# Performance work log

Hardware: AMD Instinct MI355X
Metric: run time of the kernel (lower is better)

Reference implementation:

```python
import jax, jax.numpy as jnp
import numpy as np

jax.config.update("jax_enable_x64", True)

STRIDE = 1
PADDING = 1


def _im2col(x, k, s):
    # x: (n, c, H, W) already padded. Returns (n, c*k*k, oh*ow) with
    # channel-major, then (kh, kw) ordering -- matching torch unfold/img2col.
    n, c, H, W = x.shape
    oh = (H - k) // s + 1
    ow = (W - k) // s + 1
    # k*k = 9 slices: small fixed loop over kernel offsets, fully vectorized
    # over batch/channel/spatial dims.
    patches = jnp.stack(
        [x[:, :, i:i + s * (oh - 1) + 1:s, j:j + s * (ow - 1) + 1:s]
         for i in range(k) for j in range(k)],
        axis=2,
    )  # (n, c, k*k, oh, ow)
    return patches.reshape(n, c * k * k, oh * ow)


def setup_inputs() -> dict:
    key = jax.random.key(0)
    k1, k2, k3 = jax.random.split(key, 3)
    x = jax.random.randint(k1, (32, 64, 56, 56), 0, 65536, dtype=jnp.int64)
    weight = jax.random.randint(k2, (64, 64, 3, 3), 0, 65536, dtype=jnp.int64)
    bias = jax.random.randint(k3, (64,), 0, 65536, dtype=jnp.int64)
    return {"x": x, "weight": weight, "bias": bias}


def reference(x, weight, bias):
    kN, kC, k, _ = weight.shape
    n, c, H, W = x.shape
    oh = (H - k + 2 * PADDING) // STRIDE + 1
    ow = (W - k + 2 * PADDING) // STRIDE + 1
    # pad spatial dims with zeros (ring zero)
    xp = jnp.pad(x, ((0, 0), (0, 0), (PADDING, PADDING), (PADDING, PADDING)))
    cols = _im2col(xp, k, STRIDE)              # (n, c*k*k, L)
    cols_t = cols.transpose(0, 2, 1)           # (n, L, c*k*k)
    w2 = weight.reshape(kN, kC * k * k).T      # (c*k*k, kN)
    # int64 matmul: overflow wraps (two's complement), matching ring Z_{2^64}
    out = jnp.einsum('nlk,ko->nlo', cols_t, w2) + bias  # (n, L, kN)
    return out.transpose(0, 2, 1).reshape(n, kN, oh, ow)
```

## Files before the change

kernel.cpp:

```cpp
#include <hip/hip_runtime.h>


typedef int v4i __attribute__((ext_vector_type(4)));

#define XP   (58 * 58 * 128)
#define ROWB (58 * 128)
#define LCOL 144
#define LROW (58 * LCOL)

__device__ __align__(16) unsigned char g_xp[32 * XP];
__device__ int g_sp[32 * 3364];
__device__ __align__(16) unsigned char g_wb[2 * 9 * 64 * 64];
__device__ unsigned g_off[64];

__global__ __launch_bounds__(256) void packx(const int* __restrict__ x) {
    int gid = blockIdx.x * 256 + threadIdx.x;
    if (gid >= 32 * 3364) return;
    int p = gid % 3364;
    int n = gid / 3364;
    int pr = p / 58, pc = p - pr * 58;
    int ih = pr - 1, iw = pc - 1;
    unsigned char* ob = g_xp + (long)n * XP + (long)p * 128;
    int S;
    if ((unsigned)ih < 56u && (unsigned)iw < 56u) {
        const int* xp = x + (long)n * 64 * 3136 + ih * 56 + iw;
        unsigned lo[16], hi[16];
        int s = 0;
#pragma unroll
        for (int wd = 0; wd < 16; ++wd) {
            unsigned l = 0, h = 0;
#pragma unroll
            for (int j = 0; j < 4; ++j) {
                unsigned v = (unsigned)xp[(long)(wd * 4 + j) * 3136];
                s += (int)(v & 0xFFFFu);
                l |= (((v      ) & 0xFFu) ^ 0x80u) << (8 * j);
                h |= (((v >>  8) & 0xFFu) ^ 0x80u) << (8 * j);
            }
            lo[wd] = l; hi[wd] = h;
        }
#pragma unroll
        for (int q = 0; q < 4; ++q) {
            *(uint4*)(ob + 16 * q)      = make_uint4(lo[4*q], lo[4*q+1], lo[4*q+2], lo[4*q+3]);
            *(uint4*)(ob + 64 + 16 * q) = make_uint4(hi[4*q], hi[4*q+1], hi[4*q+2], hi[4*q+3]);
        }
        S = s - 2105344;
    } else {
        uint4 v = make_uint4(0x80808080u, 0x80808080u, 0x80808080u, 0x80808080u);
#pragma unroll
        for (int q = 0; q < 4; ++q) {
            *(uint4*)(ob + 16 * q)      = v;
            *(uint4*)(ob + 64 + 16 * q) = v;
        }
        S = -2105344;
    }
    g_sp[gid] = S;
}

__global__ __launch_bounds__(256) void packw(const int* __restrict__ w,
                                             const int* __restrict__ bias) {
    int blk = blockIdx.x;
    if (blk < 144) {
        int i = blk * 256 + threadIdx.x;
        if (i >= 64 * 64 * 9) return;
        int k = i / 576;
        int r = i - k * 576;
        int c = r / 9;
        int t = r - c * 9;
        unsigned v = (unsigned)w[i];
        g_wb[((0 * 9 + t) * 64 + k) * 64 + c] = (unsigned char)((v & 255u) ^ 0x80u);
        g_wb[((1 * 9 + t) * 64 + k) * 64 + c] = (unsigned char)(((v >> 8) & 255u) ^ 0x80u);
    } else if (threadIdx.x < 64) {
        int k = threadIdx.x;
        int s0 = 0, s1 = 0;
        for (int j = 0; j < 576; ++j) {
            unsigned W = (unsigned)w[k * 576 + j];
            s0 += (int)(W & 255u);
            s1 += (int)((W >> 8) & 255u);
        }
        s0 -= 73728;
        s1 -= 73728;
        unsigned ws = (unsigned)(s0 + 256 * s1);
        g_off[k] = (unsigned)bias[k] + 32896u * ws + 1082146816u * 576u;
    }
}

__global__ __launch_bounds__(256, 2) void secconv(int* __restrict__ out) {
    __shared__ unsigned char sx[4 * LROW];
    __shared__ int ss[4 * 58];

    const int tid  = threadIdx.x;
    const int blk  = blockIdx.x;
    const int q    = blk >> 3;
    const int rp   = q % 28;
    const int n    = (blk & 7) + 8 * (q / 28);
    const int wid  = tid >> 6;
    const int lane = tid & 63;
    const int lm   = lane & 15;
    const int lq   = lane >> 4;
    const int kp   = wid & 1;
    const int ph   = wid >> 1;
    const int kbase = kp * 32;

    const unsigned char* gp = g_xp + (long)n * XP + (long)(2 * rp) * ROWB;
#pragma unroll
    for (int s = 0; s < 8; ++s) {
        int i = tid + s * 256;
        if (i < 1856) {
            uint4 v = *(const uint4*)(gp + 16 * i);
            int grow = i / 464;
            int j    = i - grow * 464;
            int gcol = j >> 3, sub = j & 7;
            *(uint4*)(sx + grow * LROW + gcol * LCOL + sub * 16) = v;
        }
    }
    if (tid < 232)
        ss[tid] = g_sp[n * 3364 + (2 * rp) * 58 + tid];

    v4i wf[2][2][9];
#pragma unroll
    for (int kt = 0; kt < 2; ++kt)
#pragma unroll
        for (int l = 0; l < 2; ++l)
#pragma unroll
            for (int t = 0; t < 9; ++t)
                wf[kt][l][t] = *(const v4i*)(g_wb +
                    ((l * 9 + t) * 64 + (kbase + kt * 16 + lm)) * 64 + lq * 16);
    unsigned offv[2][4];
#pragma unroll
    for (int kt = 0; kt < 2; ++kt)
#pragma unroll
        for (int r = 0; r < 4; ++r)
            offv[kt][r] = g_off[kbase + kt * 16 + lq * 4 + r];

    __syncthreads();

    const int r8 = lm >> 3, c8 = lm & 7;
    const unsigned char* lbase = sx + r8 * LROW + c8 * LCOL + lq * 16;

    const int t0 = ph ? 4 : 0, t1 = ph ? 7 : 4;
    for (int t = t0; t < t1; ++t) {
        const unsigned char* tb = lbase + t * 8 * LCOL;
        v4i a00[2] = {{0,0,0,0},{0,0,0,0}}, a01[2] = {{0,0,0,0},{0,0,0,0}};
        v4i a10[2] = {{0,0,0,0},{0,0,0,0}}, a11[2] = {{0,0,0,0},{0,0,0,0}};
#pragma unroll
        for (int tap = 0; tap < 9; ++tap) {
            const int dr = tap / 3, dc = tap - (tap / 3) * 3;
            const unsigned char* pp = tb + dr * LROW + dc * LCOL;
            v4i bl = *(const v4i*)(pp);
            v4i bh = *(const v4i*)(pp + 64);
#pragma unroll
            for (int kt = 0; kt < 2; ++kt) {
                a00[kt] = __builtin_amdgcn_mfma_i32_16x16x64_i8(wf[kt][0][tap], bl, a00[kt], 0, 0, 0);
                a01[kt] = __builtin_amdgcn_mfma_i32_16x16x64_i8(wf[kt][0][tap], bh, a01[kt], 0, 0, 0);
                a10[kt] = __builtin_amdgcn_mfma_i32_16x16x64_i8(wf[kt][1][tap], bl, a10[kt], 0, 0, 0);
                a11[kt] = __builtin_amdgcn_mfma_i32_16x16x64_i8(wf[kt][1][tap], bh, a11[kt], 0, 0, 0);
            }
        }

        const int pc = t * 8 + c8;
        int Q = 0;
#pragma unroll
        for (int dr = 0; dr < 3; ++dr)
#pragma unroll
            for (int dc = 0; dc < 3; ++dc)
                Q += ss[(r8 + dr) * 58 + pc + dc];
        const unsigned qq = 32896u * (unsigned)Q;

        const long pix = (long)(2 * rp + r8) * 56 + pc;
#pragma unroll
        for (int kt = 0; kt < 2; ++kt) {
            const long ob = ((long)n * 64 + kbase + kt * 16 + lq * 4) * 3136 + pix;
#pragma unroll
            for (int r = 0; r < 4; ++r) {
                unsigned val = (unsigned)a00[kt][r]
                             + (((unsigned)a01[kt][r] + (unsigned)a10[kt][r]) << 8)
                             + ((unsigned)a11[kt][r] << 16)
                             + qq + offv[kt][r];
                out[ob + (long)r * 3136] = (int)val;
            }
        }
    }
}

extern "C" void kernel_launch(void* const* d_in, const int* in_sizes, int n_in,
                              void* d_out, int out_size, void* d_ws, size_t ws_size,
                              hipStream_t stream)
{
    const int* x    = (const int*)d_in[0];
    const int* w    = (const int*)d_in[1];
    const int* bias = (const int*)d_in[2];
    int* out        = (int*)d_out;

    packx  <<<dim3(421), dim3(256), 0, stream>>>(x);
    packw  <<<dim3(145), dim3(256), 0, stream>>>(w, bias);
    secconv<<<dim3(896), dim3(256), 0, stream>>>(out);
}
```

Before: 119.4 us.

## Fuse input packing into conv kernel, packing directly into shared memory

Removes the separate packx kernel and its global staging buffers; each conv block now reads the raw input rows it needs, splits bytes with perm instructions, biases them, and writes them straight into shared memory along with per-pixel sums. This eliminates a launch and a full write/read of the packed intermediate. In exchange, halo rows are read twice across blocks and packing is done by fewer threads with strided loads, putting the load latency on the conv kernel's critical path.

```diff
diff --git a/kernel.cpp b/kernel.cpp
--- a/kernel.cpp
+++ b/kernel.cpp
@@ -3,57 +3,18 @@
 
 typedef int v4i __attribute__((ext_vector_type(4)));
 
-#define XP   (58 * 58 * 128)
-#define ROWB (58 * 128)
 #define LCOL 144
 #define LROW (58 * LCOL)
 
-__device__ __align__(16) unsigned char g_xp[32 * XP];
-__device__ int g_sp[32 * 3364];
 __device__ __align__(16) unsigned char g_wb[2 * 9 * 64 * 64];
 __device__ unsigned g_off[64];
 
-__global__ __launch_bounds__(256) void packx(const int* __restrict__ x) {
-    int gid = blockIdx.x * 256 + threadIdx.x;
-    if (gid >= 32 * 3364) return;
-    int p = gid % 3364;
-    int n = gid / 3364;
-    int pr = p / 58, pc = p - pr * 58;
-    int ih = pr - 1, iw = pc - 1;
-    unsigned char* ob = g_xp + (long)n * XP + (long)p * 128;
-    int S;
-    if ((unsigned)ih < 56u && (unsigned)iw < 56u) {
-        const int* xp = x + (long)n * 64 * 3136 + ih * 56 + iw;
-        unsigned lo[16], hi[16];
-        int s = 0;
-#pragma unroll
-        for (int wd = 0; wd < 16; ++wd) {
-            unsigned l = 0, h = 0;
-#pragma unroll
-            for (int j = 0; j < 4; ++j) {
-                unsigned v = (unsigned)xp[(long)(wd * 4 + j) * 3136];
-                s += (int)(v & 0xFFFFu);
-                l |= (((v      ) & 0xFFu) ^ 0x80u) << (8 * j);
-                h |= (((v >>  8) & 0xFFu) ^ 0x80u) << (8 * j);
-            }
-            lo[wd] = l; hi[wd] = h;
-        }
-#pragma unroll
-        for (int q = 0; q < 4; ++q) {
-            *(uint4*)(ob + 16 * q)      = make_uint4(lo[4*q], lo[4*q+1], lo[4*q+2], lo[4*q+3]);
-            *(uint4*)(ob + 64 + 16 * q) = make_uint4(hi[4*q], hi[4*q+1], hi[4*q+2], hi[4*q+3]);
-        }
-        S = s - 2105344;
-    } else {
-        uint4 v = make_uint4(0x80808080u, 0x80808080u, 0x80808080u, 0x80808080u);
-#pragma unroll
-        for (int q = 0; q < 4; ++q) {
-            *(uint4*)(ob + 16 * q)      = v;
-            *(uint4*)(ob + 64 + 16 * q) = v;
-        }
-        S = -2105344;
-    }
-    g_sp[gid] = S;
+static __device__ __forceinline__ unsigned bsum(unsigned v, unsigned acc) {
+#if __has_builtin(__builtin_amdgcn_sad_u8)
+    return __builtin_amdgcn_sad_u8(v, 0u, acc);
+#else
+    return acc + (v & 0xFFu) + ((v >> 8) & 0xFFu) + ((v >> 16) & 0xFFu) + (v >> 24);
+#endif
 }
 
 __global__ __launch_bounds__(256) void packw(const int* __restrict__ w,
@@ -84,9 +45,11 @@
     }
 }
 
-__global__ __launch_bounds__(256, 2) void secconv(int* __restrict__ out) {
+__global__ __launch_bounds__(256, 2) void secconv(const int* __restrict__ x,
+                                                  int* __restrict__ out)
+{
     __shared__ unsigned char sx[4 * LROW];
-    __shared__ int ss[4 * 58];
+    __shared__ int ss[232];
 
     const int tid  = threadIdx.x;
     const int blk  = blockIdx.x;
@@ -101,20 +64,48 @@
     const int ph   = wid >> 1;
     const int kbase = kp * 32;
 
-    const unsigned char* gp = g_xp + (long)n * XP + (long)(2 * rp) * ROWB;
+    if (tid < 232) {
+        const int pr = tid / 58, pc = tid - pr * 58;
+        const int ih = 2 * rp - 1 + pr, iw = pc - 1;
+        unsigned char* ob = sx + pr * LROW + pc * LCOL;
+        int S;
+        if ((unsigned)ih < 56u && (unsigned)iw < 56u) {
+            const int* xp = x + (long)n * 64 * 3136 + ih * 56 + iw;
+            unsigned slo = 0, shi = 0;
 #pragma unroll
-    for (int s = 0; s < 8; ++s) {
-        int i = tid + s * 256;
-        if (i < 1856) {
-            uint4 v = *(const uint4*)(gp + 16 * i);
-            int grow = i / 464;
-            int j    = i - grow * 464;
-            int gcol = j >> 3, sub = j & 7;
-            *(uint4*)(sx + grow * LROW + gcol * LCOL + sub * 16) = v;
+            for (int g = 0; g < 4; ++g) {
+                unsigned lo[4], hi[4];
+#pragma unroll
+                for (int u = 0; u < 4; ++u) {
+                    const int c = g * 16 + u * 4;
+                    unsigned v0 = (unsigned)xp[(c + 0) * 3136];
+                    unsigned v1 = (unsigned)xp[(c + 1) * 3136];
+                    unsigned v2 = (unsigned)xp[(c + 2) * 3136];
+                    unsigned v3 = (unsigned)xp[(c + 3) * 3136];
+                    unsigned t01 = __builtin_amdgcn_perm(v1, v0, 0x05040100u);
+                    unsigned t23 = __builtin_amdgcn_perm(v3, v2, 0x05040100u);
+                    unsigned lw  = __builtin_amdgcn_perm(t23, t01, 0x06040200u);
+                    unsigned hw  = __builtin_amdgcn_perm(t23, t01, 0x07050301u);
+                    slo = bsum(lw, slo);
+                    shi = bsum(hw, shi);
+                    lo[u] = lw ^ 0x80808080u;
+                    hi[u] = hw ^ 0x80808080u;
+                }
+                *(uint4*)(ob + g * 16)      = make_uint4(lo[0], lo[1], lo[2], lo[3]);
+                *(uint4*)(ob + 64 + g * 16) = make_uint4(hi[0], hi[1], hi[2], hi[3]);
+            }
+            S = (int)(slo + (shi << 8)) - 2105344;
+        } else {
+            uint4 v = make_uint4(0x80808080u, 0x80808080u, 0x80808080u, 0x80808080u);
+#pragma unroll
+            for (int g = 0; g < 4; ++g) {
+                *(uint4*)(ob + g * 16)      = v;
+                *(uint4*)(ob + 64 + g * 16) = v;
+            }
+            S = -2105344;
         }
+        ss[tid] = S;
     }
-    if (tid < 232)
-        ss[tid] = g_sp[n * 3364 + (2 * rp) * 58 + tid];
 
     v4i wf[2][2][9];
 #pragma unroll
@@ -191,7 +182,6 @@
     const int* bias = (const int*)d_in[2];
     int* out        = (int*)d_out;
 
-    packx  <<<dim3(421), dim3(256), 0, stream>>>(x);
     packw  <<<dim3(145), dim3(256), 0, stream>>>(w, bias);
-    secconv<<<dim3(896), dim3(256), 0, stream>>>(out);
+    secconv<<<dim3(896), dim3(256), 0, stream>>>(x, out);
 }
```

Result: faster. 108.7 us (-9.0%).
